# Performance work log

Measured on AMD Instinct MI355X. Metric: run time of the kernel, lower is better.

## Reference

```python
import jax, jax.numpy as jnp
import numpy as np

N = 50000
E = 600000
D_IN = 128
D_HID = 128


def gcn_conv(x, src, dst, ew, W, b):
    """PyG-style GCNConv with self-loops and symmetric normalization.
    x: [N, Fin], src/dst: [E'], ew: [E'], W: [Fin, Fout], b: [Fout].
    """
    n = x.shape[0]
    # degree from incoming edge weights (self-loops already appended)
    deg = jax.ops.segment_sum(ew, dst, num_segments=n)
    dinv = jnp.where(deg > 0, jax.lax.rsqrt(deg), 0.0)
    norm = dinv[src] * ew * dinv[dst]  # [E']
    h = x @ W  # linear transform first (PyG order)
    msg = h[src] * norm[:, None]  # gather + scale, [E', Fout]
    out = jax.ops.segment_sum(msg, dst, num_segments=n)  # scatter-add
    return out + b


def setup_inputs() -> dict:
    key = jax.random.key(0)
    k1, k2, k3, k4, k5, k6, k7 = jax.random.split(key, 7)
    x = jax.random.normal(k1, (N, D_IN), dtype=jnp.float32)
    edge_index = jax.random.randint(k2, (2, E), 0, N, dtype=jnp.int64)
    edge_weight = jax.random.uniform(k3, (E,), dtype=jnp.float32)
    s1 = 1.0 / np.sqrt(D_IN)
    s2 = 1.0 / np.sqrt(D_HID)
    W1 = jax.random.uniform(k4, (D_IN, D_HID), dtype=jnp.float32, minval=-s1, maxval=s1)
    b1 = jax.random.uniform(k5, (D_HID,), dtype=jnp.float32, minval=-s1, maxval=s1)
    W2 = jax.random.uniform(k6, (D_HID, D_IN), dtype=jnp.float32, minval=-s2, maxval=s2)
    b2 = jax.random.uniform(k7, (D_IN,), dtype=jnp.float32, minval=-s2, maxval=s2)
    return {"x": x, "edge_index": edge_index, "edge_weight": edge_weight,
            "W1": W1, "b1": b1, "W2": W2, "b2": b2}


def reference(x, edge_index, edge_weight, W1, b1, W2, b2):
    n = x.shape[0]
    loops = jnp.arange(n, dtype=edge_index.dtype)
    src = jnp.concatenate([edge_index[0], loops])
    dst = jnp.concatenate([edge_index[1], loops])
    ew = jnp.concatenate([edge_weight, jnp.ones((n,), dtype=edge_weight.dtype)])
    h = gcn_conv(x, src, dst, ew, W1, b1)
    h = jax.nn.relu(h)
    h = gcn_conv(h, src, dst, ew, W2, b2)
    return jax.nn.sigmoid(h)
```

## Files before the change

### kernel.cpp

```cpp
#include <hip/hip_runtime.h>
#include <math.h>


typedef unsigned int uint32;
typedef unsigned long long u64;
typedef __attribute__((ext_vector_type(8))) short bf16x8;
typedef __attribute__((ext_vector_type(4))) float f32x4;
typedef __attribute__((ext_vector_type(2))) float f32x2;

__device__ __forceinline__ unsigned short f2bf(float f) {
    uint32 b = __float_as_uint(f);
    return (unsigned short)((b + 0x7FFFu + ((b >> 16) & 1u)) >> 16);
}

template <int AFP32, int OUTFP8>
__device__ __forceinline__ void gemm_body(const void* __restrict__ Ap,
                                          const unsigned short* __restrict__ WT,
                                          void* __restrict__ H,
                                          int n, int tb) {
    const int lane = threadIdx.x & 63;
    const int wv   = threadIdx.x >> 6;
    const int quad = lane >> 4;
    const int l16  = lane & 15;
    const int m0   = tb * 128 + wv * 32;
    f32x4 acc[2][8] = {};

    #pragma unroll
    for (int ks = 0; ks < 4; ++ks) {
        const int k0 = ks * 32 + quad * 8;
        bf16x8 a[2];
        #pragma unroll
        for (int rt = 0; rt < 2; ++rt) {
            int row = m0 + rt * 16 + l16;
            if (row >= n) row = n - 1;
            if (AFP32) {
                const float* Af = (const float*)Ap + (size_t)row * 128 + k0;
                float4 f0 = *(const float4*)(Af);
                float4 f1 = *(const float4*)(Af + 4);
                bf16x8 v;
                v[0] = (short)f2bf(f0.x); v[1] = (short)f2bf(f0.y);
                v[2] = (short)f2bf(f0.z); v[3] = (short)f2bf(f0.w);
                v[4] = (short)f2bf(f1.x); v[5] = (short)f2bf(f1.y);
                v[6] = (short)f2bf(f1.z); v[7] = (short)f2bf(f1.w);
                a[rt] = v;
            } else {
                const unsigned short* Ab = (const unsigned short*)Ap + (size_t)row * 128 + k0;
                a[rt] = *(const bf16x8*)Ab;
            }
        }
        #pragma unroll
        for (int ct = 0; ct < 8; ++ct) {
            bf16x8 b = *(const bf16x8*)(WT + (size_t)(ct * 16 + l16) * 128 + k0);
            acc[0][ct] = __builtin_amdgcn_mfma_f32_16x16x32_bf16(a[0], b, acc[0][ct], 0, 0, 0);
            acc[1][ct] = __builtin_amdgcn_mfma_f32_16x16x32_bf16(a[1], b, acc[1][ct], 0, 0, 0);
        }
    }

    #pragma unroll
    for (int rt = 0; rt < 2; ++rt) {
        #pragma unroll
        for (int r = 0; r < 4; ++r) {
            int row = m0 + rt * 16 + quad * 4 + r;
            if (row < n) {
                if (OUTFP8) {
                    unsigned char* o = (unsigned char*)H + (size_t)row * 128 + l16;
                    #pragma unroll
                    for (int cp = 0; cp < 4; ++cp) {
                        int pk = __builtin_amdgcn_cvt_pk_fp8_f32(
                            acc[rt][2 * cp][r], acc[rt][2 * cp + 1][r], 0, false);
                        o[(2 * cp) * 16]     = (unsigned char)(pk & 0xFF);
                        o[(2 * cp + 1) * 16] = (unsigned char)((pk >> 8) & 0xFF);
                    }
                } else {
                    unsigned short* o = (unsigned short*)H + (size_t)row * 128 + l16;
                    #pragma unroll
                    for (int ct = 0; ct < 8; ++ct)
                        o[ct * 16] = f2bf(acc[rt][ct][r]);
                }
            }
        }
    }
}

__global__ __launch_bounds__(256) void k_init(u64* __restrict__ packed, int n4,
                                              int* __restrict__ done,
                                              const float* __restrict__ W1,
                                              const float* __restrict__ W2,
                                              unsigned short* __restrict__ WT1,
                                              unsigned short* __restrict__ WT2) {
    int idx = blockIdx.x * 256 + threadIdx.x;
    if (idx < n4) ((uint4*)packed)[idx] = make_uint4(0u, 0u, 0u, 0u);
    if (idx == 0) *done = 0;
    if (blockIdx.x < 64) {
        int j = blockIdx.x * 256 + threadIdx.x;
        int k = j >> 7, nn = j & 127;
        WT1[nn * 128 + k] = f2bf(W1[k * 128 + nn]);
        WT2[nn * 128 + k] = f2bf(W2[k * 128 + nn]);
    }
}

__global__ __launch_bounds__(256) void k_gemm1_hist(const float* __restrict__ x,
                                                    const unsigned short* __restrict__ WT1,
                                                    unsigned char* __restrict__ h8,
                                                    const int* __restrict__ dst,
                                                    const float* __restrict__ ew,
                                                    u64* __restrict__ packed,
                                                    int* __restrict__ rank,
                                                    int E, int N, int gGemm) {
    const int b = blockIdx.x;
    if (b < gGemm) {
        gemm_body<1, 1>(x, WT1, h8, N, b);
        return;
    }
    int i = (b - gGemm) * 256 + threadIdx.x;
    if (i < E) {
        int d = dst[i];
        int r = (i >> 8) & 7;
        u64 add = (1ULL << 44) + (u64)(ew[i] * 4294967296.0f);
        u64 old = atomicAdd(&packed[(size_t)r * N + d], add);
        rank[i] = (int)(old >> 44);
    }
}

__global__ __launch_bounds__(256) void k_scan(const u64* __restrict__ packed,
                                              float* __restrict__ dinv,
                                              u64* __restrict__ bases,
                                              int* __restrict__ rowptr,
                                              int* __restrict__ csums,
                                              int* __restrict__ done, int nNodes) {
    __shared__ int s[256];
    __shared__ int lastFlag;
    const int t = threadIdx.x;
    const int base = blockIdx.x * 1024 + t * 4;
    const int n = nNodes + 1;
    int v[4];
    #pragma unroll
    for (int u = 0; u < 4; ++u) {
        int idx = base + u;
        int c = 0;
        if (idx < nNodes) {
            const u64 mask = (1ULL << 44) - 1;
            u64 ssum = 0;
            u64 bs = 0;
            uint32 cum = 0;
            #pragma unroll
            for (int r = 0; r < 8; ++r) {
                u64 pv = packed[(size_t)r * nNodes + idx];
                bs |= (u64)cum << (8 * r);
                cum += (uint32)(pv >> 44);
                ssum += (pv & mask);
            }
            c = (int)cum;
            float deg = 1.0f + (float)ssum * (1.0f / 4294967296.0f);
            dinv[idx] = rsqrtf(deg);
            bases[idx] = bs;
        }
        v[u] = c;
    }
    s[t] = v[0] + v[1] + v[2] + v[3];
    __syncthreads();
    #pragma unroll
    for (int off = 1; off < 256; off <<= 1) {
        int x = (t >= off) ? s[t - off] : 0;
        __syncthreads();
        s[t] += x;
        __syncthreads();
    }
    if (t == 255)
        __hip_atomic_store(&csums[blockIdx.x], s[255], __ATOMIC_RELEASE,
                           __HIP_MEMORY_SCOPE_AGENT);
    int e = (t == 0) ? 0 : s[t - 1];
    if (base + 0 < n) rowptr[base + 0] = e;
    if (base + 1 < n) rowptr[base + 1] = e + v[0];
    if (base + 2 < n) rowptr[base + 2] = e + v[0] + v[1];
    if (base + 3 < n) rowptr[base + 3] = e + v[0] + v[1] + v[2];

    __syncthreads();
    if (t == 0) {
        int prev = __hip_atomic_fetch_add(done, 1, __ATOMIC_ACQ_REL,
                                          __HIP_MEMORY_SCOPE_AGENT);
        lastFlag = (prev == (int)gridDim.x - 1);
    }
    __syncthreads();
    if (lastFlag && t < 64) {
        int g = (int)gridDim.x;
        int orig = (t < g) ? __hip_atomic_load(&csums[t], __ATOMIC_ACQUIRE,
                                               __HIP_MEMORY_SCOPE_AGENT)
                           : 0;
        int vv = orig;
        #pragma unroll
        for (int off = 1; off < 64; off <<= 1) {
            int y = __shfl_up(vv, off, 64);
            if (t >= off) vv += y;
        }
        if (t < g) csums[t] = vv - orig;
    }
}

__global__ __launch_bounds__(256) void k_fill(const int* __restrict__ src,
                                              const int* __restrict__ dst,
                                              const float* __restrict__ ew,
                                              const float* __restrict__ dinv,
                                              const int* __restrict__ rowptr,
                                              const int* __restrict__ csums,
                                              const u64* __restrict__ bases,
                                              const int* __restrict__ rank,
                                              float2* __restrict__ csr, int e) {
    int i = blockIdx.x * 256 + threadIdx.x;
    if (i < e) {
        int s = src[i], d = dst[i];
        int r = (i >> 8) & 7;
        float nrm = dinv[s] * ew[i] * dinv[d];
        int pos = rowptr[d] + csums[d >> 10]
                + (int)((bases[d] >> (8 * r)) & 0xFF) + rank[i];
        csr[pos] = make_float2(__int_as_float(s), nrm);
    }
}

__device__ __forceinline__ void fma8_f8(float* acc, uint2 u, float w) {
    f32x2 f;
    f = __builtin_amdgcn_cvt_pk_f32_fp8((int)u.x, false);
    acc[0] += f[0] * w; acc[1] += f[1] * w;
    f = __builtin_amdgcn_cvt_pk_f32_fp8((int)u.x, true);
    acc[2] += f[0] * w; acc[3] += f[1] * w;
    f = __builtin_amdgcn_cvt_pk_f32_fp8((int)u.y, false);
    acc[4] += f[0] * w; acc[5] += f[1] * w;
    f = __builtin_amdgcn_cvt_pk_f32_fp8((int)u.y, true);
    acc[6] += f[0] * w; acc[7] += f[1] * w;
}

__device__ __forceinline__ void gather_q8(float* acc, const uint2* __restrict__ T,
                                          const float2* __restrict__ csr,
                                          int start, int end, int l) {
    for (int k = start; k < end; k += 8) {
        float2 c[8];
        float w[8];
        uint2 u[8];
        #pragma unroll
        for (int j = 0; j < 8; ++j) {
            int ej = k + j;
            c[j] = csr[ej < end ? ej : end - 1];
            w[j] = (ej < end) ? c[j].y : 0.0f;
        }
        #pragma unroll
        for (int j = 0; j < 8; ++j)
            u[j] = T[(size_t)__float_as_int(c[j].x) * 16 + l];
        #pragma unroll
        for (int j = 0; j < 8; ++j) fma8_f8(acc, u[j], w[j]);
    }
}

__global__ __launch_bounds__(256) void k_ag1(const unsigned char* __restrict__ h8,
                                             const float2* __restrict__ csr,
                                             const int* __restrict__ rowptr,
                                             const int* __restrict__ csums,
                                             const float* __restrict__ dinv,
                                             const float4* __restrict__ bias4,
                                             unsigned char* __restrict__ g8, int N) {
    const int lane = threadIdx.x & 63;
    const int q = lane >> 4, l = lane & 15;
    const int node = blockIdx.x * 16 + (threadIdx.x >> 6) * 4 + q;
    if (node >= N) return;
    const uint2* H2 = (const uint2*)h8;
    const int start = rowptr[node] + csums[node >> 10];
    const int end   = rowptr[node + 1] + csums[(node + 1) >> 10];
    const float di = dinv[node];

    float acc[8] = {};
    fma8_f8(acc, H2[(size_t)node * 16 + l], di * di);
    gather_q8(acc, H2, csr, start, end, l);

    float4 b0 = bias4[l * 2], b1v = bias4[l * 2 + 1];
    acc[0] += b0.x;  acc[1] += b0.y;  acc[2] += b0.z;  acc[3] += b0.w;
    acc[4] += b1v.x; acc[5] += b1v.y; acc[6] += b1v.z; acc[7] += b1v.w;
    #pragma unroll
    for (int j = 0; j < 8; ++j) acc[j] = fmaxf(acc[j], 0.0f);
    uint2 o;
    int w0 = __builtin_amdgcn_cvt_pk_fp8_f32(acc[0], acc[1], 0, false);
    w0     = __builtin_amdgcn_cvt_pk_fp8_f32(acc[2], acc[3], w0, true);
    int w1 = __builtin_amdgcn_cvt_pk_fp8_f32(acc[4], acc[5], 0, false);
    w1     = __builtin_amdgcn_cvt_pk_fp8_f32(acc[6], acc[7], w1, true);
    o.x = (uint32)w0; o.y = (uint32)w1;
    ((uint2*)g8)[(size_t)node * 16 + l] = o;
}

__global__ __launch_bounds__(256) void k_ag2s(const unsigned char* __restrict__ g8,
                                              const float2* __restrict__ csr,
                                              const int* __restrict__ rowptr,
                                              const int* __restrict__ csums,
                                              const float* __restrict__ dinv,
                                              const float* __restrict__ b2,
                                              const unsigned short* __restrict__ WT2,
                                              float* __restrict__ out, int N) {
    __shared__ unsigned short sA[16][136];
    const int lane = threadIdx.x & 63;
    const int wv   = threadIdx.x >> 6;
    const int q    = lane >> 4;
    const int l    = lane & 15;
    const int nb   = blockIdx.x * 16;
    const int node = nb + wv * 4 + q;
    const uint2* G2 = (const uint2*)g8;

    float acc[8] = {};
    if (node < N) {
        const int start = rowptr[node] + csums[node >> 10];
        const int end   = rowptr[node + 1] + csums[(node + 1) >> 10];
        const float di = dinv[node];
        fma8_f8(acc, G2[(size_t)node * 16 + l], di * di);
        gather_q8(acc, G2, csr, start, end, l);
    }
    uint4 o = make_uint4(0u, 0u, 0u, 0u);
    if (node < N) {
        o.x = (uint32)f2bf(acc[0]) | ((uint32)f2bf(acc[1]) << 16);
        o.y = (uint32)f2bf(acc[2]) | ((uint32)f2bf(acc[3]) << 16);
        o.z = (uint32)f2bf(acc[4]) | ((uint32)f2bf(acc[5]) << 16);
        o.w = (uint32)f2bf(acc[6]) | ((uint32)f2bf(acc[7]) << 16);
    }
    *(uint4*)&sA[wv * 4 + q][l * 8] = o;

    __syncthreads();

    f32x4 a2[2] = {};
    #pragma unroll
    for (int ks = 0; ks < 4; ++ks) {
        const int k0 = ks * 32 + q * 8;
        bf16x8 a = *(const bf16x8*)&sA[l][k0];
        #pragma unroll
        for (int ct = 0; ct < 2; ++ct) {
            bf16x8 b = *(const bf16x8*)(WT2 + (size_t)(wv * 32 + ct * 16 + l) * 128 + k0);
            a2[ct] = __builtin_amdgcn_mfma_f32_16x16x32_bf16(a, b, a2[ct], 0, 0, 0);
        }
    }
    #pragma unroll
    for (int ct = 0; ct < 2; ++ct) {
        const int col = wv * 32 + ct * 16 + l;
        const float bb = b2[col];
        #pragma unroll
        for (int r = 0; r < 4; ++r) {
            int row = nb + q * 4 + r;
            if (row < N) {
                float v = a2[ct][r] + bb;
                out[(size_t)row * 128 + col] = 1.0f / (1.0f + expf(-v));
            }
        }
    }
}

extern "C" void kernel_launch(void* const* d_in, const int* in_sizes, int n_in,
                              void* d_out, int out_size, void* d_ws, size_t ws_size,
                              hipStream_t stream) {
    const float* x  = (const float*)d_in[0];
    const int*   ei = (const int*)d_in[1];
    const float* ew = (const float*)d_in[2];
    const float* W1 = (const float*)d_in[3];
    const float* b1 = (const float*)d_in[4];
    const float* W2 = (const float*)d_in[5];
    const float* b2 = (const float*)d_in[6];

    const int N = in_sizes[0] / 128;
    const int E = in_sizes[2];
    const int* src = ei;
    const int* dst = ei + E;
    float* out = (float*)d_out;

    auto align = [](size_t v) { return (v + 255) & ~(size_t)255; };
    char* p = (char*)d_ws;
    float*  dinv   = (float*)p;   p += align((size_t)N * 4);
    int*    rowptr = (int*)p;     p += align((size_t)(N + 1) * 4);
    int*    csums  = (int*)p;     p += align((size_t)1024 * 4);
    int*    done   = (int*)p;     p += align((size_t)256);
    u64*    bases  = (u64*)p;     p += align((size_t)N * 8);
    unsigned short* WT1 = (unsigned short*)p; p += align((size_t)128 * 128 * 2);
    unsigned short* WT2 = (unsigned short*)p; p += align((size_t)128 * 128 * 2);
    int*    rank   = (int*)p;     p += align((size_t)E * 4);
    float2* csr    = (float2*)p;  p += align((size_t)E * 8);
    unsigned char*  h8 = (unsigned char*)p;  p += align((size_t)N * 128);
    unsigned char*  g8 = (unsigned char*)p;
    u64* packed = (u64*)g8;

    const int nbE = (E + 255) / 256;
    const int gScan = (N + 1 + 1023) / 1024;
    const int gGemm = (N + 127) / 128;
    const int gAg1  = (N + 15) / 16;
    const int gAg2  = (N + 15) / 16;
    const int n4 = N * 4;
    const int gInit = ((n4 + 255) / 256) < 64 ? 64 : ((n4 + 255) / 256);

    k_init<<<gInit, 256, 0, stream>>>(packed, n4, done, W1, W2, WT1, WT2);
    k_gemm1_hist<<<gGemm + nbE, 256, 0, stream>>>(x, WT1, h8, dst, ew, packed,
                                                  rank, E, N, gGemm);
    k_scan<<<gScan, 256, 0, stream>>>(packed, dinv, bases, rowptr, csums, done, N);
    k_fill<<<nbE, 256, 0, stream>>>(src, dst, ew, dinv, rowptr, csums, bases,
                                    rank, csr, E);

    k_ag1<<<gAg1, 256, 0, stream>>>(h8, csr, rowptr, csums, dinv,
                                    (const float4*)b1, g8, N);

    k_ag2s<<<gAg2, 256, 0, stream>>>(g8, csr, rowptr, csums, dinv, b2,
                                     WT2, out, N);
}
```

Before: 190.2 us.

## Replace rank-based deterministic CSR fill with atomic per-node cursor

The histogram pass no longer uses 8 replicated counter banks with returned ranks. It now does a single non-returning atomic per edge into one packed counter per node. The fill kernel gets each edge's slot from an atomicAdd on a per-node cursor, so the rank and bases arrays and their reads and writes go away. In exchange, edge order within each CSR row is nondeterministic, so float accumulation order can change between runs. Contention on the per-node counters may also rise.

```diff
diff --git a/kernel.cpp b/kernel.cpp
--- a/kernel.cpp
+++ b/kernel.cpp
@@ -82,14 +82,15 @@
     }
 }
 
-__global__ __launch_bounds__(256) void k_init(u64* __restrict__ packed, int n4,
+__global__ __launch_bounds__(256) void k_init(u64* __restrict__ packed,
+                                              int* __restrict__ cnt, int n,
                                               int* __restrict__ done,
                                               const float* __restrict__ W1,
                                               const float* __restrict__ W2,
                                               unsigned short* __restrict__ WT1,
                                               unsigned short* __restrict__ WT2) {
     int idx = blockIdx.x * 256 + threadIdx.x;
-    if (idx < n4) ((uint4*)packed)[idx] = make_uint4(0u, 0u, 0u, 0u);
+    if (idx < n) { packed[idx] = 0ULL; cnt[idx] = 0; }
     if (idx == 0) *done = 0;
     if (blockIdx.x < 64) {
         int j = blockIdx.x * 256 + threadIdx.x;
@@ -105,7 +106,6 @@
                                                     const int* __restrict__ dst,
                                                     const float* __restrict__ ew,
                                                     u64* __restrict__ packed,
-                                                    int* __restrict__ rank,
                                                     int E, int N, int gGemm) {
     const int b = blockIdx.x;
     if (b < gGemm) {
@@ -115,16 +115,13 @@
     int i = (b - gGemm) * 256 + threadIdx.x;
     if (i < E) {
         int d = dst[i];
-        int r = (i >> 8) & 7;
         u64 add = (1ULL << 44) + (u64)(ew[i] * 4294967296.0f);
-        u64 old = atomicAdd(&packed[(size_t)r * N + d], add);
-        rank[i] = (int)(old >> 44);
+        atomicAdd(&packed[d], add);
     }
 }
 
 __global__ __launch_bounds__(256) void k_scan(const u64* __restrict__ packed,
                                               float* __restrict__ dinv,
-                                              u64* __restrict__ bases,
                                               int* __restrict__ rowptr,
                                               int* __restrict__ csums,
                                               int* __restrict__ done, int nNodes) {
@@ -140,20 +137,10 @@
         int c = 0;
         if (idx < nNodes) {
             const u64 mask = (1ULL << 44) - 1;
-            u64 ssum = 0;
-            u64 bs = 0;
-            uint32 cum = 0;
-            #pragma unroll
-            for (int r = 0; r < 8; ++r) {
-                u64 pv = packed[(size_t)r * nNodes + idx];
-                bs |= (u64)cum << (8 * r);
-                cum += (uint32)(pv >> 44);
-                ssum += (pv & mask);
-            }
-            c = (int)cum;
-            float deg = 1.0f + (float)ssum * (1.0f / 4294967296.0f);
+            u64 pv = packed[idx];
+            c = (int)(pv >> 44);
+            float deg = 1.0f + (float)(pv & mask) * (1.0f / 4294967296.0f);
             dinv[idx] = rsqrtf(deg);
-            bases[idx] = bs;
         }
         v[u] = c;
     }
@@ -203,16 +190,13 @@
                                               const float* __restrict__ dinv,
                                               const int* __restrict__ rowptr,
                                               const int* __restrict__ csums,
-                                              const u64* __restrict__ bases,
-                                              const int* __restrict__ rank,
+                                              int* __restrict__ cnt,
                                               float2* __restrict__ csr, int e) {
     int i = blockIdx.x * 256 + threadIdx.x;
     if (i < e) {
         int s = src[i], d = dst[i];
-        int r = (i >> 8) & 7;
         float nrm = dinv[s] * ew[i] * dinv[d];
-        int pos = rowptr[d] + csums[d >> 10]
-                + (int)((bases[d] >> (8 * r)) & 0xFF) + rank[i];
+        int pos = rowptr[d] + csums[d >> 10] + atomicAdd(&cnt[d], 1);
         csr[pos] = make_float2(__int_as_float(s), nrm);
     }
 }
@@ -369,29 +353,28 @@
     int*    rowptr = (int*)p;     p += align((size_t)(N + 1) * 4);
     int*    csums  = (int*)p;     p += align((size_t)1024 * 4);
     int*    done   = (int*)p;     p += align((size_t)256);
-    u64*    bases  = (u64*)p;     p += align((size_t)N * 8);
     unsigned short* WT1 = (unsigned short*)p; p += align((size_t)128 * 128 * 2);
     unsigned short* WT2 = (unsigned short*)p; p += align((size_t)128 * 128 * 2);
-    int*    rank   = (int*)p;     p += align((size_t)E * 4);
     float2* csr    = (float2*)p;  p += align((size_t)E * 8);
     unsigned char*  h8 = (unsigned char*)p;  p += align((size_t)N * 128);
     unsigned char*  g8 = (unsigned char*)p;
     u64* packed = (u64*)g8;
+    int* cnt    = (int*)(g8 + align((size_t)N * 8));
 
     const int nbE = (E + 255) / 256;
     const int gScan = (N + 1 + 1023) / 1024;
     const int gGemm = (N + 127) / 128;
     const int gAg1  = (N + 15) / 16;
     const int gAg2  = (N + 15) / 16;
-    const int n4 = N * 4;
-    const int gInit = ((n4 + 255) / 256) < 64 ? 64 : ((n4 + 255) / 256);
-
-    k_init<<<gInit, 256, 0, stream>>>(packed, n4, done, W1, W2, WT1, WT2);
+    const int gInit0 = (N + 255) / 256;
+    const int gInit = gInit0 < 64 ? 64 : gInit0;
+
+    k_init<<<gInit, 256, 0, stream>>>(packed, cnt, N, done, W1, W2, WT1, WT2);
     k_gemm1_hist<<<gGemm + nbE, 256, 0, stream>>>(x, WT1, h8, dst, ew, packed,
-                                                  rank, E, N, gGemm);
-    k_scan<<<gScan, 256, 0, stream>>>(packed, dinv, bases, rowptr, csums, done, N);
-    k_fill<<<nbE, 256, 0, stream>>>(src, dst, ew, dinv, rowptr, csums, bases,
-                                    rank, csr, E);
+                                                  E, N, gGemm);
+    k_scan<<<gScan, 256, 0, stream>>>(packed, dinv, rowptr, csums, done, N);
+    k_fill<<<nbE, 256, 0, stream>>>(src, dst, ew, dinv, rowptr, csums, cnt,
+                                    csr, E);
 
     k_ag1<<<gAg1, 256, 0, stream>>>(h8, csr, rowptr, csums, dinv,
                                     (const float4*)b1, g8, N);
```

New measurement: 208.0 us. +9.4%, slower.
